# Kernel tuning notes

Hardware: AMD Instinct MI355X
Metric: run time of the kernel (lower is better)

## Reference

```python
import jax, jax.numpy as jnp
import numpy as np

IGNORE_INDEX = -100
BETA = 0.1

B, T, H, V = 4, 512, 1024, 32000  # sequences, tokens/seq, hidden, vocab


def setup_inputs() -> dict:
    key = jax.random.key(0)
    ks = jax.random.split(key, 9)
    scale = 1.0 / np.sqrt(H)
    return {
        "_input": jax.random.normal(ks[0], (B * T, H), jnp.float32),
        "weight": jax.random.normal(ks[1], (V, H), jnp.float32) * scale,
        "target": jax.random.randint(ks[2], (B * T,), 0, V, jnp.int64),
        "bias": jax.random.normal(ks[3], (V,), jnp.float32) * 0.01,
        "preference_labels": jax.random.bernoulli(ks[4], 0.5, (B,)),
        "ref_input": jax.random.normal(ks[5], (B * T, H), jnp.float32),
        "ref_weight": jax.random.normal(ks[6], (V, H), jnp.float32) * scale,
        "ref_bias": jax.random.normal(ks[7], (V,), jnp.float32) * 0.01,
        "kl": jax.random.uniform(ks[8], (1,), jnp.float32),
    }


def _seq_log_prob(x, w, b, target):
    # x: (B*T, H), w: (V, H), b: (V,) -> per-sequence summed target logprob (B,)
    logits = x @ w.T + b  # (B*T, V) -- the tensor the fused kernel avoids
    logp = jax.nn.log_softmax(logits, axis=-1)
    safe_tgt = jnp.clip(target, 0, logp.shape[-1] - 1)
    tok_logp = jnp.take_along_axis(logp, safe_tgt[:, None], axis=-1)[:, 0]
    mask = target != IGNORE_INDEX
    tok_logp = jnp.where(mask, tok_logp, 0.0).reshape(B, T)
    return tok_logp.sum(axis=-1)  # average_log_prob=False


def reference(_input, weight, target, bias, preference_labels, ref_input, ref_weight, ref_bias, kl):
    pol_logp = _seq_log_prob(_input, weight, bias, target)          # (B,)
    ref_logp = _seq_log_prob(ref_input, ref_weight, ref_bias, target)  # (B,)
    logratios = pol_logp - ref_logp
    multiplier = jnp.where(preference_labels, 1.0, -1.0)
    losses = 1.0 - jax.nn.sigmoid(BETA * (logratios - kl[0]) * multiplier)
    loss = losses.sum() / target.shape[0]  # divide by full_target.shape[0] = B*T
    rewards = BETA * logratios
    chosen_rewards_sum = (rewards * preference_labels).sum()
    rejected_rewards_sum = (rewards * (~preference_labels)).sum()
    return loss, chosen_rewards_sum, rejected_rewards_sum
```

## Files before the change

kernel.cpp:

```cpp
#include <hip/hip_runtime.h>

#define BT    2048
#define HDIM  1024
#define VDIM  32000
#define NSEQ  4
#define BETA  0.1f
#define IGNORE_IDX (-100)

typedef __attribute__((ext_vector_type(8))) short bf16x8;
typedef __attribute__((ext_vector_type(8))) unsigned short u16x8;
typedef __attribute__((ext_vector_type(4))) float f32x4;

#define WS_BF_BYTE  32768
#define XBF_OFF     0
#define XRBF_OFF    (BT * HDIM)
#define WBF_OFF     (2 * BT * HDIM)
#define WRBF_OFF    (2 * BT * HDIM + VDIM * HDIM)
#define CVT_TOTAL   (2 * BT * HDIM + 2 * VDIM * HDIM)
#define WS_NEED     ((size_t)WS_BF_BYTE + (size_t)CVT_TOTAL * 2)

__device__ __forceinline__ unsigned short f2bf_rne(float f) {
  unsigned int u = __builtin_bit_cast(unsigned int, f);
  u += 0x7fffu + ((u >> 16) & 1u);
  return (unsigned short)(u >> 16);
}

__device__ __forceinline__ u16x8 cvt8(float4 a, float4 b) {
  u16x8 v;
  v[0] = f2bf_rne(a.x); v[1] = f2bf_rne(a.y); v[2] = f2bf_rne(a.z); v[3] = f2bf_rne(a.w);
  v[4] = f2bf_rne(b.x); v[5] = f2bf_rne(b.y); v[6] = f2bf_rne(b.z); v[7] = f2bf_rne(b.w);
  return v;
}

__global__ __launch_bounds__(256) void kto_zero_ws(float* p) {
  p[blockIdx.x * 256 + threadIdx.x] = 0.0f;
}

__global__ __launch_bounds__(256) void kto_convert(
    const float* __restrict__ X, const float* __restrict__ Xr,
    const float* __restrict__ W, const float* __restrict__ Wr,
    unsigned short* __restrict__ bf)
{
  size_t gid8 = ((size_t)blockIdx.x * 256 + threadIdx.x) * 8;
  if (gid8 >= (size_t)CVT_TOTAL) return;
  const float* src; size_t off;
  if (gid8 < (size_t)XRBF_OFF)      { src = X;  off = gid8; }
  else if (gid8 < (size_t)WBF_OFF)  { src = Xr; off = gid8 - XRBF_OFF; }
  else if (gid8 < (size_t)WRBF_OFF) { src = W;  off = gid8 - WBF_OFF; }
  else                              { src = Wr; off = gid8 - WRBF_OFF; }
  const float4* p = (const float4*)(src + off);
  float4 a = p[0], b = p[1];
  *(u16x8*)(bf + gid8) = cvt8(a, b);
}

#define GLD16(g, l) __builtin_amdgcn_global_load_lds( \
    (const __attribute__((address_space(1))) unsigned int*)(g), \
    (__attribute__((address_space(3))) unsigned int*)(l), 16, 0, 0)

__global__ __launch_bounds__(512, 2) void kto_lse_gemm_fast(
    const unsigned short* __restrict__ bf,
    const float* __restrict__ Bp, const float* __restrict__ Br,
    const int* __restrict__ target,
    float* __restrict__ ws_se, float* __restrict__ ws_tg)
{
  const int model = blockIdx.z;
  const unsigned short* __restrict__ Xb = bf + (model ? XRBF_OFF : XBF_OFF);
  const unsigned short* __restrict__ Wb = bf + (model ? WRBF_OFF : WBF_OFF);
  const float* __restrict__ Bv = model ? Br : Bp;

  const int lin  = blockIdx.x + (blockIdx.y << 3);
  const int wgid = (lin & 7) * 125 + (lin >> 3);
  const int mBase = (wgid & 7) * 256;
  const int nBase = (wgid >> 3) * 256;

  __shared__ unsigned short lds[4 * 16384];

  const int tid  = threadIdx.x;
  const int wave = tid >> 6;
  const int lane = tid & 63;
  const int q    = lane >> 4;
  const int c    = lane & 15;
  const int wm   = wave >> 2;
  const int wn   = wave & 3;

  const int lrow = lane >> 2;
  const int lchk = (lane & 3) ^ ((lane >> 3) & 3);

  const char* gsrc[4];
  int ldst[4];
  #pragma unroll
  for (int j = 0; j < 4; ++j) {
    const int seg = wave * 4 + j;
    if (seg < 16) {
      const int row = mBase + seg * 16 + lrow;
      gsrc[j] = (const char*)Xb + (size_t)row * (HDIM * 2) + lchk * 16;
      ldst[j] = seg * 512;
    } else {
      const int row = nBase + (seg - 16) * 16 + lrow;
      gsrc[j] = (const char*)Wb + (size_t)row * (HDIM * 2) + lchk * 16;
      ldst[j] = 8192 + (seg - 16) * 512;
    }
  }

  #pragma unroll
  for (int u = 0; u < 2; ++u) {
    unsigned short* dst = &lds[u * 16384];
    #pragma unroll
    for (int j = 0; j < 4; ++j)
      GLD16(gsrc[j] + u * 64, &dst[ldst[j]]);
  }
  asm volatile("s_waitcnt vmcnt(4)" ::: "memory");
  __builtin_amdgcn_s_barrier();

  const int swz   = (q ^ ((c >> 1) & 3)) * 8;
  const int aBase = (wm * 128 + c) * 32 + swz;
  const int bBase = 8192 + (wn * 64 + c) * 32 + swz;

  f32x4 acc[8][4] = {};

  for (int u = 0; u < 32; ++u) {
    const unsigned short* sl = &lds[(u & 3) * 16384];
    unsigned short* dst = &lds[((u + 2) & 3) * 16384];
    const int kb2 = ((u + 2) & 31) * 64;

    bf16x8 afr[4], bfr[4];
    #pragma unroll
    for (int ni = 0; ni < 4; ++ni)
      bfr[ni] = *(const bf16x8*)&sl[bBase + ni * 512];
    #pragma unroll
    for (int mi = 0; mi < 4; ++mi)
      afr[mi] = *(const bf16x8*)&sl[aBase + mi * 512];
    GLD16(gsrc[0] + kb2, &dst[ldst[0]]);
    GLD16(gsrc[1] + kb2, &dst[ldst[1]]);
    __builtin_amdgcn_s_barrier();
    asm volatile("s_waitcnt lgkmcnt(0)" ::: "memory");
    __builtin_amdgcn_sched_barrier(0);
    __builtin_amdgcn_s_setprio(1);
    #pragma unroll
    for (int mi = 0; mi < 4; ++mi)
      #pragma unroll
      for (int ni = 0; ni < 4; ++ni)
        acc[mi][ni] = __builtin_amdgcn_mfma_f32_16x16x32_bf16(afr[mi], bfr[ni], acc[mi][ni], 0, 0, 0);
    __builtin_amdgcn_s_setprio(0);
    __builtin_amdgcn_s_barrier();

    #pragma unroll
    for (int mi = 0; mi < 4; ++mi)
      afr[mi] = *(const bf16x8*)&sl[aBase + 2048 + mi * 512];
    GLD16(gsrc[2] + kb2, &dst[ldst[2]]);
    GLD16(gsrc[3] + kb2, &dst[ldst[3]]);
    asm volatile("s_waitcnt vmcnt(4)" ::: "memory");
    __builtin_amdgcn_s_barrier();
    asm volatile("s_waitcnt lgkmcnt(0)" ::: "memory");
    __builtin_amdgcn_sched_barrier(0);
    __builtin_amdgcn_s_setprio(1);
    #pragma unroll
    for (int mi = 0; mi < 4; ++mi)
      #pragma unroll
      for (int ni = 0; ni < 4; ++ni)
        acc[mi + 4][ni] = __builtin_amdgcn_mfma_f32_16x16x32_bf16(afr[mi], bfr[ni], acc[mi + 4][ni], 0, 0, 0);
    __builtin_amdgcn_s_setprio(0);
    __builtin_amdgcn_s_barrier();
  }

  float bv[4]; int colc[4];
  #pragma unroll
  for (int ni = 0; ni < 4; ++ni) {
    colc[ni] = nBase + wn * 64 + ni * 16 + c;
    bv[ni] = Bv[colc[ni]];
  }

  #pragma unroll
  for (int mi = 0; mi < 8; ++mi) {
    const int rowb = mBase + wm * 128 + mi * 16 + q * 4;
    int tgt4[4];
    #pragma unroll
    for (int r = 0; r < 4; ++r) tgt4[r] = target[rowb + r];
    float se[4] = {0.f, 0.f, 0.f, 0.f};
    float tg[4] = {0.f, 0.f, 0.f, 0.f};
    #pragma unroll
    for (int ni = 0; ni < 4; ++ni)
      #pragma unroll
      for (int r = 0; r < 4; ++r) {
        float logit = acc[mi][ni][r] + bv[ni];
        se[r] += __expf(logit);
        if (tgt4[r] == colc[ni]) tg[r] += logit;
      }
    #pragma unroll
    for (int r = 0; r < 4; ++r) {
      float s = se[r];
      float t = tg[r];
      #pragma unroll
      for (int off = 1; off < 16; off <<= 1) {
        s += __shfl_xor(s, off, 64);
        t += __shfl_xor(t, off, 64);
      }
      if (c == ((mi * 4 + r) & 15)) {
        const int row = rowb + r;
        atomicAdd(&ws_se[model * BT + row], s);
        atomicAdd(&ws_tg[model * BT + row], t);
      }
    }
  }
}

#define SBM 128
#define SBN 128
#define SBK 32
#define SVSLICE 1280
#define SNITER  (SVSLICE / SBN)
#define SKTILES (HDIM / SBK)
#define SLDK    (SBK + 8)

__device__ __forceinline__ void cvt_store8s(unsigned short* dst, float4 a, float4 b) {
  *(u16x8*)dst = cvt8(a, b);
}

__global__ __launch_bounds__(256) void kto_lse_gemm_slow(
    const float* __restrict__ Xp, const float* __restrict__ Wp, const float* __restrict__ Bp,
    const float* __restrict__ Xr, const float* __restrict__ Wr, const float* __restrict__ Br,
    const int* __restrict__ target, float* __restrict__ ws_se, float* __restrict__ ws_tg)
{
  const int model = blockIdx.z;
  const float* __restrict__ X  = model ? Xr : Xp;
  const float* __restrict__ W  = model ? Wr : Wp;
  const float* __restrict__ Bv = model ? Br : Bp;

  __shared__ unsigned short Asm[SBM][SLDK];
  __shared__ unsigned short Bsm[SBN][SLDK];

  const int tid  = threadIdx.x;
  const int wave = tid >> 6;
  const int lane = tid & 63;
  const int q    = lane >> 4;
  const int c    = lane & 15;
  const int mW   = (wave >> 1) * 64;
  const int nW   = (wave & 1) * 64;
  const int mBase = blockIdx.x * SBM;
  const int vBase = blockIdx.y * SVSLICE;

  const int srow = tid >> 1;
  const int scol = (tid & 1) << 4;

  int tgt_idx[4][4];
  #pragma unroll
  for (int mi = 0; mi < 4; ++mi)
    #pragma unroll
    for (int r = 0; r < 4; ++r)
      tgt_idx[mi][r] = target[mBase + mW + mi * 16 + q * 4 + r];

  float se_acc[4][4] = {};
  float tg_acc[4][4] = {};

  for (int it = 0; it < SNITER; ++it) {
    const int nIterBase = vBase + it * SBN;
    f32x4 acc[4][4] = {};

    for (int kt = 0; kt < SKTILES; ++kt) {
      __syncthreads();
      {
        const float4* a4 = (const float4*)(X + (size_t)(mBase + srow) * HDIM + kt * SBK + scol);
        float4 a0 = a4[0], a1 = a4[1], a2 = a4[2], a3 = a4[3];
        const float4* b4 = (const float4*)(W + (size_t)(nIterBase + srow) * HDIM + kt * SBK + scol);
        float4 b0 = b4[0], b1 = b4[1], b2 = b4[2], b3 = b4[3];
        cvt_store8s(&Asm[srow][scol],     a0, a1);
        cvt_store8s(&Asm[srow][scol + 8], a2, a3);
        cvt_store8s(&Bsm[srow][scol],     b0, b1);
        cvt_store8s(&Bsm[srow][scol + 8], b2, b3);
      }
      __syncthreads();

      bf16x8 afr[4], bfr[4];
      #pragma unroll
      for (int mi = 0; mi < 4; ++mi)
        afr[mi] = *(const bf16x8*)&Asm[mW + mi * 16 + c][q * 8];
      #pragma unroll
      for (int ni = 0; ni < 4; ++ni)
        bfr[ni] = *(const bf16x8*)&Bsm[nW + ni * 16 + c][q * 8];
      #pragma unroll
      for (int mi = 0; mi < 4; ++mi)
        #pragma unroll
        for (int ni = 0; ni < 4; ++ni)
          acc[mi][ni] = __builtin_amdgcn_mfma_f32_16x16x32_bf16(afr[mi], bfr[ni], acc[mi][ni], 0, 0, 0);
    }

    #pragma unroll
    for (int ni = 0; ni < 4; ++ni) {
      const int col = nIterBase + nW + ni * 16 + c;
      const float bv = Bv[col];
      #pragma unroll
      for (int mi = 0; mi < 4; ++mi)
        #pragma unroll
        for (int r = 0; r < 4; ++r) {
          float logit = acc[mi][ni][r] + bv;
          se_acc[mi][r] += __expf(logit);
          if (tgt_idx[mi][r] == col) tg_acc[mi][r] += logit;
        }
    }
  }

  #pragma unroll
  for (int mi = 0; mi < 4; ++mi)
    #pragma unroll
    for (int r = 0; r < 4; ++r) {
      float s = se_acc[mi][r];
      float t = tg_acc[mi][r];
      #pragma unroll
      for (int off = 1; off < 16; off <<= 1) {
        s += __shfl_xor(s, off, 64);
        t += __shfl_xor(t, off, 64);
      }
      if (c == 0) {
        const int row = mBase + mW + mi * 16 + q * 4 + r;
        atomicAdd(&ws_se[model * BT + row], s);
        atomicAdd(&ws_tg[model * BT + row], t);
      }
    }
}

__global__ __launch_bounds__(256) void kto_finalize(
    const float* __restrict__ ws_se, const float* __restrict__ ws_tg,
    const int* __restrict__ target, const int* __restrict__ pref,
    const float* __restrict__ kl, float* __restrict__ out)
{
  __shared__ float lr[NSEQ];
  const int tid = threadIdx.x;
  if (tid < NSEQ) lr[tid] = 0.0f;
  __syncthreads();
  for (int t = tid; t < BT; t += 256) {
    float d = 0.0f;
    if (target[t] != IGNORE_IDX) {
      float lp_p = ws_tg[t]      - __logf(ws_se[t]);
      float lp_r = ws_tg[BT + t] - __logf(ws_se[BT + t]);
      d = lp_p - lp_r;
    }
    atomicAdd(&lr[t >> 9], d);
  }
  __syncthreads();
  if (tid == 0) {
    float loss = 0.f, ch = 0.f, rj = 0.f;
    const float klv = kl[0];
    for (int b = 0; b < NSEQ; ++b) {
      float logratio = lr[b];
      bool p = pref[b] != 0;
      float mult = p ? 1.0f : -1.0f;
      float z = BETA * (logratio - klv) * mult;
      float sig = 1.0f / (1.0f + __expf(-z));
      loss += 1.0f - sig;
      float rw = BETA * logratio;
      if (p) ch += rw; else rj += rw;
    }
    out[0] = loss / (float)BT;
    out[1] = ch;
    out[2] = rj;
  }
}

extern "C" void kernel_launch(void* const* d_in, const int* in_sizes, int n_in,
                              void* d_out, int out_size, void* d_ws, size_t ws_size,
                              hipStream_t stream) {
  (void)in_sizes; (void)n_in; (void)out_size;
  const float* X    = (const float*)d_in[0];
  const float* W    = (const float*)d_in[1];
  const int*   tgt  = (const int*)d_in[2];
  const float* bias = (const float*)d_in[3];
  const int*   pref = (const int*)d_in[4];
  const float* Xr   = (const float*)d_in[5];
  const float* Wr   = (const float*)d_in[6];
  const float* br   = (const float*)d_in[7];
  const float* kl   = (const float*)d_in[8];
  float* out = (float*)d_out;

  float* ws_se = (float*)d_ws;
  float* ws_tg = ws_se + 2 * BT;

  kto_zero_ws<<<32, 256, 0, stream>>>(ws_se);

  if (ws_size >= WS_NEED) {
    unsigned short* bf = (unsigned short*)((char*)d_ws + WS_BF_BYTE);
    kto_convert<<<(CVT_TOTAL / 2048), 256, 0, stream>>>(X, Xr, W, Wr, bf);
    dim3 grid(BT / 256, VDIM / 256, 2);
    kto_lse_gemm_fast<<<grid, 512, 0, stream>>>(bf, bias, br, tgt, ws_se, ws_tg);
  } else {
    dim3 grid(BT / SBM, VDIM / SVSLICE, 2);
    kto_lse_gemm_slow<<<grid, 256, 0, stream>>>(X, W, bias, Xr, Wr, br, tgt, ws_se, ws_tg);
  }

  kto_finalize<<<1, 256, 0, stream>>>(ws_se, ws_tg, tgt, pref, kl, out);
}
```

Measured before the change: 615.0 us.

## Deepen GEMM pipeline to three stages with register double-buffered A fragments

Restructures the K loop of the fused logits GEMM. It prefetches three LDS stages instead of two, uses one barrier per iteration instead of four, and double-buffers the A-operand fragments in registers so the next step's A loads overlap the current MFMAs. The loop is fully unrolled and the MFMA order is switched to ni-outer. The aim is to cut barrier and LDS-wait stalls in the main loop, at the cost of more VGPRs (two sets of eight A fragments) and a risk of lower occupancy or register spills.

```diff
diff --git a/kernel.cpp b/kernel.cpp
--- a/kernel.cpp
+++ b/kernel.cpp
@@ -102,65 +102,58 @@
     }
   }
 
-  #pragma unroll
-  for (int u = 0; u < 2; ++u) {
-    unsigned short* dst = &lds[u * 16384];
-    #pragma unroll
-    for (int j = 0; j < 4; ++j)
-      GLD16(gsrc[j] + u * 64, &dst[ldst[j]]);
-  }
-  asm volatile("s_waitcnt vmcnt(4)" ::: "memory");
-  __builtin_amdgcn_s_barrier();
-
   const int swz   = (q ^ ((c >> 1) & 3)) * 8;
   const int aBase = (wm * 128 + c) * 32 + swz;
   const int bBase = 8192 + (wn * 64 + c) * 32 + swz;
 
+  #pragma unroll
+  for (int u = 0; u < 3; ++u) {
+    unsigned short* dst = &lds[u * 16384];
+    #pragma unroll
+    for (int j = 0; j < 4; ++j)
+      GLD16(gsrc[j] + u * 64, &dst[ldst[j]]);
+  }
+  asm volatile("s_waitcnt vmcnt(8)" ::: "memory");
+  __builtin_amdgcn_s_barrier();
+
+  bf16x8 fA[2][8];
+  #pragma unroll
+  for (int mi = 0; mi < 8; ++mi)
+    fA[0][mi] = *(const bf16x8*)&lds[aBase + mi * 512];
+
   f32x4 acc[8][4] = {};
 
+  #pragma unroll
   for (int u = 0; u < 32; ++u) {
-    const unsigned short* sl = &lds[(u & 3) * 16384];
-    unsigned short* dst = &lds[((u + 2) & 3) * 16384];
-    const int kb2 = ((u + 2) & 31) * 64;
-
-    bf16x8 afr[4], bfr[4];
-    #pragma unroll
-    for (int ni = 0; ni < 4; ++ni)
-      bfr[ni] = *(const bf16x8*)&sl[bBase + ni * 512];
-    #pragma unroll
-    for (int mi = 0; mi < 4; ++mi)
-      afr[mi] = *(const bf16x8*)&sl[aBase + mi * 512];
-    GLD16(gsrc[0] + kb2, &dst[ldst[0]]);
-    GLD16(gsrc[1] + kb2, &dst[ldst[1]]);
-    __builtin_amdgcn_s_barrier();
-    asm volatile("s_waitcnt lgkmcnt(0)" ::: "memory");
-    __builtin_amdgcn_sched_barrier(0);
-    __builtin_amdgcn_s_setprio(1);
-    #pragma unroll
-    for (int mi = 0; mi < 4; ++mi)
-      #pragma unroll
-      for (int ni = 0; ni < 4; ++ni)
-        acc[mi][ni] = __builtin_amdgcn_mfma_f32_16x16x32_bf16(afr[mi], bfr[ni], acc[mi][ni], 0, 0, 0);
-    __builtin_amdgcn_s_setprio(0);
-    __builtin_amdgcn_s_barrier();
-
-    #pragma unroll
-    for (int mi = 0; mi < 4; ++mi)
-      afr[mi] = *(const bf16x8*)&sl[aBase + 2048 + mi * 512];
-    GLD16(gsrc[2] + kb2, &dst[ldst[2]]);
-    GLD16(gsrc[3] + kb2, &dst[ldst[3]]);
     asm volatile("s_waitcnt vmcnt(4)" ::: "memory");
     __builtin_amdgcn_s_barrier();
-    asm volatile("s_waitcnt lgkmcnt(0)" ::: "memory");
-    __builtin_amdgcn_sched_barrier(0);
+
+    unsigned short* dst = &lds[((u + 3) & 3) * 16384];
+    const size_t kb = (size_t)((u + 3) & 31) * 64;
+    #pragma unroll
+    for (int j = 0; j < 4; ++j)
+      GLD16(gsrc[j] + kb, &dst[ldst[j]]);
+
+    const unsigned short* slC = &lds[(u & 3) * 16384];
+    bf16x8 fB[4];
+    #pragma unroll
+    for (int ni = 0; ni < 4; ++ni)
+      fB[ni] = *(const bf16x8*)&slC[bBase + ni * 512];
+
+    if (u < 31) {
+      const unsigned short* slN = &lds[((u + 1) & 3) * 16384];
+      #pragma unroll
+      for (int mi = 0; mi < 8; ++mi)
+        fA[(u + 1) & 1][mi] = *(const bf16x8*)&slN[aBase + mi * 512];
+    }
+
     __builtin_amdgcn_s_setprio(1);
     #pragma unroll
-    for (int mi = 0; mi < 4; ++mi)
-      #pragma unroll
-      for (int ni = 0; ni < 4; ++ni)
-        acc[mi + 4][ni] = __builtin_amdgcn_mfma_f32_16x16x32_bf16(afr[mi], bfr[ni], acc[mi + 4][ni], 0, 0, 0);
+    for (int ni = 0; ni < 4; ++ni)
+      #pragma unroll
+      for (int mi = 0; mi < 8; ++mi)
+        acc[mi][ni] = __builtin_amdgcn_mfma_f32_16x16x32_bf16(fA[u & 1][mi], fB[ni], acc[mi][ni], 0, 0, 0);
     __builtin_amdgcn_s_setprio(0);
-    __builtin_amdgcn_s_barrier();
   }
 
   float bv[4]; int colc[4];
```

Result: slower. 632.7 us (+2.9%).
